# Kernel tuning notes

Measured on AMD Instinct MI355X. Metric: run time of the kernel, lower is better.

Reference implementation:

```python
import jax, jax.numpy as jnp
import numpy as np

B, S, T = 4, 512, 512
V, D, F, H, DK, N = 32000, 512, 2048, 8, 64, 6
PAD = 0

# sinusoidal positional encoding table, matching the torch source exactly
_pos = np.arange(max(S, T))[:, None]
_i = np.arange(D // 2)[None, :]
_ang = _pos / (10000.0 ** (2 * _i / D))
_pe = np.empty((max(S, T), D), dtype=np.float32)
_pe[:, 0::2] = np.sin(_ang)
_pe[:, 1::2] = np.cos(_ang)
PE = jnp.asarray(_pe)


def setup_inputs() -> dict:
    key = jax.random.key(0)
    ks = iter(jax.random.split(key, 64))
    s = 0.02
    w = lambda shape: jax.random.normal(next(ks), shape, jnp.float32) * s
    inp = {
        'src': jax.random.randint(next(ks), (B, S), 0, V, jnp.int32),
        'trg': jax.random.randint(next(ks), (B, T), 0, V, jnp.int32),
        'emb_src': w((V, D)).at[PAD].set(0.0),
        'emb_trg': w((V, D)).at[PAD].set(0.0),
        # encoder stacks (leading axis = layer)
        'enc_wq': w((N, D, H * DK)), 'enc_wk': w((N, D, H * DK)),
        'enc_wv': w((N, D, H * DK)), 'enc_wo': w((N, H * DK, D)),
        'enc_ln1_g': jnp.ones((N, D)), 'enc_ln1_b': jnp.zeros((N, D)),
        'enc_w1': w((N, D, F)), 'enc_b1': jnp.zeros((N, F)),
        'enc_w2': w((N, F, D)), 'enc_b2': jnp.zeros((N, D)),
        'enc_ln2_g': jnp.ones((N, D)), 'enc_ln2_b': jnp.zeros((N, D)),
        # decoder stacks
        'dec_wq': w((N, D, H * DK)), 'dec_wk': w((N, D, H * DK)),
        'dec_wv': w((N, D, H * DK)), 'dec_wo': w((N, H * DK, D)),
        'dec_ln1_g': jnp.ones((N, D)), 'dec_ln1_b': jnp.zeros((N, D)),
        'dec_cq': w((N, D, H * DK)), 'dec_ck': w((N, D, H * DK)),
        'dec_cv': w((N, D, H * DK)), 'dec_co': w((N, H * DK, D)),
        'dec_ln2_g': jnp.ones((N, D)), 'dec_ln2_b': jnp.zeros((N, D)),
        'dec_w1': w((N, D, F)), 'dec_b1': jnp.zeros((N, F)),
        'dec_w2': w((N, F, D)), 'dec_b2': jnp.zeros((N, D)),
        'dec_ln3_g': jnp.ones((N, D)), 'dec_ln3_b': jnp.zeros((N, D)),
        'proj': w((D, V)),
    }
    return inp


def _ln(x, g, b, eps=1e-5):
    m = x.mean(-1, keepdims=True)
    v = ((x - m) ** 2).mean(-1, keepdims=True)
    return (x - m) * jax.lax.rsqrt(v + eps) * g + b


def _mha(xq, xkv, wq, wk, wv, wo, mask):
    b, lq, _ = xq.shape
    lk = xkv.shape[1]
    q = (xq @ wq).reshape(b, lq, H, DK).transpose(0, 2, 1, 3)   # bhqd
    k = (xkv @ wk).reshape(b, lk, H, DK).transpose(0, 2, 1, 3)  # bhkd
    v = (xkv @ wv).reshape(b, lk, H, DK).transpose(0, 2, 1, 3)  # bhkd
    scores = jnp.einsum('bhqd,bhkd->bhqk', q, k)
    scores = jnp.where(mask, -jnp.inf, scores)
    attn = jax.nn.softmax(scores * (DK ** -0.5), axis=-1)
    out = jnp.einsum('bhqk,bhkd->bhqd', attn, v)
    out = out.transpose(0, 2, 1, 3).reshape(b, lq, H * DK)
    return out @ wo


def _ffn(x, w1, b1, w2, b2):
    return jax.nn.relu(x @ w1 + b1) @ w2 + b2


def reference(src, trg, emb_src, emb_trg,
              enc_wq, enc_wk, enc_wv, enc_wo, enc_ln1_g, enc_ln1_b,
              enc_w1, enc_b1, enc_w2, enc_b2, enc_ln2_g, enc_ln2_b,
              dec_wq, dec_wk, dec_wv, dec_wo, dec_ln1_g, dec_ln1_b,
              dec_cq, dec_ck, dec_cv, dec_co, dec_ln2_g, dec_ln2_b,
              dec_w1, dec_b1, dec_w2, dec_b2, dec_ln3_g, dec_ln3_b,
              proj):
    scale = D ** 0.5
    src_pad = (src == PAD)[:, None, None, :]                 # [B,1,1,S]
    trg_pad = (trg == PAD)[:, None, None, :]                 # [B,1,1,T]
    causal = jnp.triu(jnp.ones((T, T), bool), 1)[None, None]  # [1,1,T,T]
    trg_mask = trg_pad | causal

    # encoder (dropout = identity in eval)
    x = emb_src[src] * scale + PE[None, :S]

    def enc_step(h, p):
        wq, wk, wv, wo, g1, b1, w1, bb1, w2, bb2, g2, b2 = p
        h = _ln(h + _mha(h, h, wq, wk, wv, wo, src_pad), g1, b1)
        h = _ln(h + _ffn(h, w1, bb1, w2, bb2), g2, b2)
        return h, None

    x_enc, _ = jax.lax.scan(enc_step, x,
        (enc_wq, enc_wk, enc_wv, enc_wo, enc_ln1_g, enc_ln1_b,
         enc_w1, enc_b1, enc_w2, enc_b2, enc_ln2_g, enc_ln2_b))

    # decoder
    y = emb_trg[trg] * scale + PE[None, :T]

    def dec_step(h, p):
        (wq, wk, wv, wo, g1, b1, cq, ck, cv, co, g2, b2,
         w1, bb1, w2, bb2, g3, b3) = p
        h = _ln(h + _mha(h, h, wq, wk, wv, wo, trg_mask), g1, b1)
        h = _ln(h + _mha(h, x_enc, cq, ck, cv, co, src_pad), g2, b2)
        h = _ln(h + _ffn(h, w1, bb1, w2, bb2), g3, b3)
        return h, None

    y, _ = jax.lax.scan(dec_step, y,
        (dec_wq, dec_wk, dec_wv, dec_wo, dec_ln1_g, dec_ln1_b,
         dec_cq, dec_ck, dec_cv, dec_co, dec_ln2_g, dec_ln2_b,
         dec_w1, dec_b1, dec_w2, dec_b2, dec_ln3_g, dec_ln3_b))

    return y @ proj  # [B, T, trg_vocab]
```

## Files before the change

### kernel.cpp

```cpp
#include <hip/hip_runtime.h>
#include <math.h>

#define BBATCH 4
#define SS 512
#define DDIM 512
#define FFN 2048
#define NHEAD 8
#define DHEAD 64
#define NL 6
#define NVOC 32000
#define MTOK (BBATCH*SS)
#define PAD_ID 0
#define MSZE ((size_t)MTOK * DDIM)

typedef unsigned short u16;
typedef __attribute__((ext_vector_type(8))) short short8;
typedef __attribute__((ext_vector_type(4))) float f32x4;

__device__ __forceinline__ u16 f2bf(float f) {
    union { float f; unsigned u; } v; v.f = f;
    unsigned r = ((v.u >> 16) & 1u) + 0x7fffu;
    return (u16)((v.u + r) >> 16);
}

__device__ __forceinline__ void gload16(const u16* g, u16* l) {
    __builtin_amdgcn_global_load_lds(
        (const __attribute__((address_space(1))) void*)g,
        (__attribute__((address_space(3))) void*)l, 16, 0, 0);
}

template<int N> __device__ __forceinline__ void waitv() {
    if constexpr (N == 0)      asm volatile("s_waitcnt vmcnt(0)" ::: "memory");
    else if constexpr (N == 2) asm volatile("s_waitcnt vmcnt(2)" ::: "memory");
    else if constexpr (N == 4) asm volatile("s_waitcnt vmcnt(4)" ::: "memory");
    else if constexpr (N == 8) asm volatile("s_waitcnt vmcnt(8)" ::: "memory");
    __builtin_amdgcn_sched_barrier(0);
}
__device__ __forceinline__ void rawbar() {
    __builtin_amdgcn_s_barrier();
    __builtin_amdgcn_sched_barrier(0);
}

template<int BM, int BN, int OUTBF, int RELU, int BIAS>
__device__ __forceinline__ void gemm_core(
    u16* __restrict__ AsB, u16* __restrict__ BsB,
    const u16* __restrict__ A, int lda,
    const u16* __restrict__ B, int ldb,
    void* __restrict__ Cv, int ldc,
    int row0, int col0, int K, const float* __restrict__ bias)
{
    const int tid  = threadIdx.x;
    const int lane = tid & 63;
    const int wid  = tid >> 6;
    const int wr   = wid >> 1, wc = wid & 1;
    constexpr int MF = BM / 32, NF = BN / 32, RA = BM / 64, RB = BN / 64;
    constexpr int LPT = RA + RB;

    const u16* aSrc[RA]; int aOff[RA];
    #pragma unroll
    for (int r = 0; r < RA; r++) {
        int row = (tid >> 2) + r * 64;
        int slot = ((tid & 3) << 4) ^ ((row & 3) << 4);
        aSrc[r] = A + (size_t)(row0 + row) * lda + (slot >> 1);
        aOff[r] = r * 2048 + tid * 8;
    }
    const u16* bSrc[RB]; int bOff[RB];
    #pragma unroll
    for (int r = 0; r < RB; r++) {
        int row = (tid >> 2) + r * 64;
        int slot = ((tid & 3) << 4) ^ ((row & 3) << 4);
        bSrc[r] = B + (size_t)(col0 + row) * ldb + (slot >> 1);
        bOff[r] = r * 2048 + tid * 8;
    }

    f32x4 acc[MF][NF];
    const f32x4 zero = {0.f, 0.f, 0.f, 0.f};
    #pragma unroll
    for (int m = 0; m < MF; m++)
        #pragma unroll
        for (int n = 0; n < NF; n++) acc[m][n] = zero;

    auto issue = [&](int t) {
        u16* ad = AsB + (t & 3) * (BM * 32);
        u16* bd = BsB + (t & 3) * (BN * 32);
        #pragma unroll
        for (int r = 0; r < RA; r++) gload16(aSrc[r] + t * 32, ad + aOff[r]);
        #pragma unroll
        for (int r = 0; r < RB; r++) gload16(bSrc[r] + t * 32, bd + bOff[r]);
    };
    auto comp = [&](int t) {
        const u16* as = AsB + (t & 3) * (BM * 32);
        const u16* bs = BsB + (t & 3) * (BN * 32);
        short8 af[MF], bf[NF];
        #pragma unroll
        for (int m = 0; m < MF; m++) {
            int row = wr * (BM / 2) + m * 16 + (lane & 15);
            int slot = ((lane >> 4) << 4) ^ ((row & 3) << 4);
            af[m] = *(const short8*)&as[row * 32 + (slot >> 1)];
        }
        #pragma unroll
        for (int n = 0; n < NF; n++) {
            int row = wc * (BN / 2) + n * 16 + (lane & 15);
            int slot = ((lane >> 4) << 4) ^ ((row & 3) << 4);
            bf[n] = *(const short8*)&bs[row * 32 + (slot >> 1)];
        }
        __builtin_amdgcn_s_setprio(1);
        #pragma unroll
        for (int m = 0; m < MF; m++)
            #pragma unroll
            for (int n = 0; n < NF; n++)
                acc[m][n] = __builtin_amdgcn_mfma_f32_16x16x32_bf16(af[m], bf[n], acc[m][n], 0, 0, 0);
        __builtin_amdgcn_s_setprio(0);
    };

    const int nt = K / 32;
    issue(0); issue(1); issue(2);
    int t = 0;
    for (; t < nt - 2; ++t) {
        waitv<2 * LPT>();
        rawbar();
        if (t + 3 < nt) issue(t + 3);
        comp(t);
    }
    waitv<LPT>(); rawbar(); comp(nt - 2);
    waitv<0>();   rawbar(); comp(nt - 1);

    const int crow = row0 + wr * (BM / 2);
    const int ccol = col0 + wc * (BN / 2);
    #pragma unroll
    for (int m = 0; m < MF; m++) {
        #pragma unroll
        for (int n = 0; n < NF; n++) {
            int col = ccol + n * 16 + (lane & 15);
            float bv = BIAS ? bias[col] : 0.0f;
            #pragma unroll
            for (int i = 0; i < 4; i++) {
                int row = crow + m * 16 + ((lane >> 4) << 2) + i;
                float v = acc[m][n][i] + bv;
                if (RELU) v = fmaxf(v, 0.0f);
                if (OUTBF) ((u16*)Cv)[(size_t)row * ldc + col] = f2bf(v);
                else       ((float*)Cv)[(size_t)row * ldc + col] = v;
            }
        }
    }
}

template<int BM, int BN, int OUTBF, int RELU, int BIAS, int SWZ = 0>
__global__ __launch_bounds__(256) void mgemm(
    const u16* __restrict__ A, int lda, size_t aSb, size_t aSh,
    const u16* __restrict__ B, int ldb, size_t bSb, size_t bSh,
    void* __restrict__ Cv, int ldc, size_t cSb, size_t cSh,
    int K, const float* __restrict__ bias)
{
    __shared__ __align__(16) u16 As[4 * BM * 32];
    __shared__ __align__(16) u16 Bs[4 * BN * 32];
    int bx = blockIdx.x, by = blockIdx.y;
    if (SWZ) {
        int nwg = gridDim.x * gridDim.y;
        int lin = by * gridDim.x + bx;
        int cpx = nwg >> 3;
        int s = (lin & 7) * cpx + (lin >> 3);
        bx = s % gridDim.x; by = s / gridDim.x;
    }
    const int zb = blockIdx.z >> 3, zh = blockIdx.z & 7;
    const u16* Ab = A + (size_t)zb * aSb + (size_t)zh * aSh;
    const u16* Bb = B + (size_t)zb * bSb + (size_t)zh * bSh;
    void* Cb = OUTBF ? (void*)((u16*)Cv + (size_t)zb * cSb + (size_t)zh * cSh)
                     : (void*)((float*)Cv + (size_t)zb * cSb + (size_t)zh * cSh);
    gemm_core<BM, BN, OUTBF, RELU, BIAS>(As, Bs, Ab, lda, Bb, ldb, Cb, ldc,
                                          by * BM, bx * BN, K, bias);
}

template<int BM, int BN>
__global__ __launch_bounds__(256) void mgemm_dual(
    const u16* __restrict__ A1, int lda1, const u16* __restrict__ B1, int ldb1,
    u16* __restrict__ C1, int ldc1, int nx1, int nblk1,
    const u16* __restrict__ A2, int lda2, const u16* __restrict__ B2, int ldb2,
    u16* __restrict__ C2, int ldc2, int nx2,
    int K)
{
    __shared__ __align__(16) u16 As[4 * BM * 32];
    __shared__ __align__(16) u16 Bs[4 * BN * 32];
    int id = blockIdx.x;
    if (id < nblk1) {
        gemm_core<BM, BN, 1, 0, 0>(As, Bs, A1, lda1, B1, ldb1, C1, ldc1,
                                    (id / nx1) * BM, (id % nx1) * BN, K, nullptr);
    } else {
        id -= nblk1;
        gemm_core<BM, BN, 1, 0, 0>(As, Bs, A2, lda2, B2, ldb2, C2, ldc2,
                                    (id / nx2) * BM, (id % nx2) * BN, K, nullptr);
    }
}

template<int CAUSAL>
__global__ __launch_bounds__(256) void flash_attn(
    const u16* __restrict__ Qp, int ldq,
    const u16* __restrict__ Kp, int ldk,
    const u16* __restrict__ Vtp,
    u16* __restrict__ O,
    const int* __restrict__ ids)
{
    __shared__ __align__(16) u16 Kl[3][64 * 64];
    __shared__ __align__(16) u16 Vl[3][64 * 64];
    __shared__ __align__(16) u16 Pl[4][16 * 64];
    __shared__ float msk[SS];

    const int tid = threadIdx.x, lane = tid & 63, wid = tid >> 6;
    const int qt = blockIdx.x, bh = blockIdx.y;
    const int b = bh >> 3, h = bh & 7;
    const int q0 = qt * 64;

    for (int i = tid; i < SS; i += 256)
        msk[i] = (ids[b * SS + i] == PAD_ID) ? -1e30f : 0.0f;

    const int qloc = wid * 16 + (lane & 15);
    const u16* Qb = Qp + (size_t)(b * SS + q0 + qloc) * ldq + h * 64 + ((lane >> 4) * 8);
    short8 qf[2];
    qf[0] = *(const short8*)(Qb);
    qf[1] = *(const short8*)(Qb + 32);

    const u16* Kb = Kp + (size_t)b * SS * ldk + h * 64;
    const u16* Vb = Vtp + (size_t)(h * 64) * MTOK + b * SS;

    auto stage = [&](int buf, int kt) {
        int row = tid >> 3, sl = tid & 7;
        #pragma unroll
        for (int r = 0; r < 2; r++) {
            int rr = row + r * 32;
            int ls = sl ^ (rr & 7);
            gload16(Kb + (size_t)(kt * 64 + rr) * ldk + ls * 8, &Kl[buf][rr * 64 + sl * 8]);
            gload16(Vb + (size_t)rr * MTOK + kt * 64 + ls * 8, &Vl[buf][rr * 64 + sl * 8]);
        }
    };

    const int nt = CAUSAL ? (qt + 1) : (SS / 64);

    float m_i[4], l_i[4];
    f32x4 o_acc[4];
    const f32x4 zero = {0.f, 0.f, 0.f, 0.f};
    #pragma unroll
    for (int i = 0; i < 4; i++) { m_i[i] = -1e30f; l_i[i] = 0.0f; }
    #pragma unroll
    for (int n = 0; n < 4; n++) o_acc[n] = zero;

    auto comp = [&](int kt) {
        const int cur = kt % 3;
        f32x4 s_acc[4];
        #pragma unroll
        for (int n = 0; n < 4; n++) s_acc[n] = zero;
        __builtin_amdgcn_s_setprio(1);
        #pragma unroll
        for (int kk = 0; kk < 2; kk++) {
            #pragma unroll
            for (int n = 0; n < 4; n++) {
                int row = n * 16 + (lane & 15);
                int ls = (kk * 4 + (lane >> 4)) ^ (row & 7);
                short8 kf = *(const short8*)&Kl[cur][row * 64 + ls * 8];
                s_acc[n] = __builtin_amdgcn_mfma_f32_16x16x32_bf16(qf[kk], kf, s_acc[n], 0, 0, 0);
            }
        }
        __builtin_amdgcn_s_setprio(0);

        float sv[4][4];
        #pragma unroll
        for (int n = 0; n < 4; n++) {
            int kg = kt * 64 + n * 16 + (lane & 15);
            float mk = msk[kg];
            #pragma unroll
            for (int i = 0; i < 4; i++) {
                float s = s_acc[n][i] * 0.125f + mk;
                if (CAUSAL) {
                    int qg = q0 + wid * 16 + ((lane >> 4) << 2) + i;
                    if (kg > qg) s = -1e30f;
                }
                sv[n][i] = s;
            }
        }
        float pm[4], mn[4], rs[4], ps[4];
        #pragma unroll
        for (int i = 0; i < 4; i++)
            pm[i] = fmaxf(fmaxf(sv[0][i], sv[1][i]), fmaxf(sv[2][i], sv[3][i]));
        #pragma unroll
        for (int i = 0; i < 4; i++) {
            #pragma unroll
            for (int msh = 1; msh <= 8; msh <<= 1)
                pm[i] = fmaxf(pm[i], __shfl_xor(pm[i], msh));
            mn[i] = fmaxf(m_i[i], pm[i]);
            rs[i] = __expf(m_i[i] - mn[i]);
            m_i[i] = mn[i];
        }
        float p[4][4];
        #pragma unroll
        for (int n = 0; n < 4; n++)
            #pragma unroll
            for (int i = 0; i < 4; i++)
                p[n][i] = (sv[n][i] < -1e29f) ? 0.0f : __expf(sv[n][i] - mn[i]);
        #pragma unroll
        for (int i = 0; i < 4; i++) {
            ps[i] = p[0][i] + p[1][i] + p[2][i] + p[3][i];
            #pragma unroll
            for (int msh = 1; msh <= 8; msh <<= 1)
                ps[i] += __shfl_xor(ps[i], msh);
            l_i[i] = l_i[i] * rs[i] + ps[i];
        }
        #pragma unroll
        for (int n = 0; n < 4; n++)
            #pragma unroll
            for (int i = 0; i < 4; i++)
                o_acc[n][i] *= rs[i];

        #pragma unroll
        for (int n = 0; n < 4; n++) {
            int k = n * 16 + (lane & 15);
            #pragma unroll
            for (int i = 0; i < 4; i++) {
                int q = ((lane >> 4) << 2) + i;
                Pl[wid][q * 64 + (((k >> 3) ^ (q & 7)) << 3) + (k & 7)] = f2bf(p[n][i]);
            }
        }
        asm volatile("s_waitcnt lgkmcnt(0)" ::: "memory");
        __builtin_amdgcn_sched_barrier(0);

        __builtin_amdgcn_s_setprio(1);
        #pragma unroll
        for (int kk = 0; kk < 2; kk++) {
            int qrow = lane & 15;
            int lsp = (kk * 4 + (lane >> 4)) ^ (qrow & 7);
            short8 pa = *(const short8*)&Pl[wid][qrow * 64 + lsp * 8];
            #pragma unroll
            for (int nf = 0; nf < 4; nf++) {
                int row = nf * 16 + (lane & 15);
                int vs = (kk * 4 + (lane >> 4)) ^ (row & 7);
                short8 vf = *(const short8*)&Vl[cur][row * 64 + vs * 8];
                o_acc[nf] = __builtin_amdgcn_mfma_f32_16x16x32_bf16(pa, vf, o_acc[nf], 0, 0, 0);
            }
        }
        __builtin_amdgcn_s_setprio(0);
    };

    stage(0, 0);
    stage(1, 1);
    int t = 0;
    for (; t < nt - 1; ++t) {
        waitv<4>();
        rawbar();
        if (t + 2 < nt) stage((t + 2) % 3, t + 2);
        comp(t);
    }
    waitv<0>(); rawbar(); comp(nt - 1);

    #pragma unroll
    for (int nf = 0; nf < 4; nf++) {
        int d = h * 64 + nf * 16 + (lane & 15);
        #pragma unroll
        for (int i = 0; i < 4; i++) {
            int qg = b * SS + q0 + wid * 16 + ((lane >> 4) << 2) + i;
            O[(size_t)qg * DDIM + d] = f2bf(o_acc[nf][i] / l_i[i]);
        }
    }
}

__device__ __forceinline__ void transp_core(const float* __restrict__ src, u16* __restrict__ dst,
                                            int N, int K, int n0, int k0)
{
    __shared__ u16 t[64][65];
    const int tid = threadIdx.x;
    #pragma unroll
    for (int i = 0; i < 16; i++) {
        int idx = tid + i * 256;
        int kr = idx >> 6, nc = idx & 63;
        t[kr][nc] = f2bf(src[(size_t)(k0 + kr) * N + n0 + nc]);
    }
    __syncthreads();
    #pragma unroll
    for (int i = 0; i < 16; i++) {
        int idx = tid + i * 256;
        int nr = idx >> 6, kc = idx & 63;
        dst[(size_t)(n0 + nr) * K + k0 + kc] = t[kc][nr];
    }
}

__global__ __launch_bounds__(256) void transp(const float* __restrict__ src, u16* __restrict__ dst,
                                              int N, int K, size_t sStride, size_t dStride)
{
    transp_core(src + (size_t)blockIdx.z * sStride, dst + (size_t)blockIdx.z * dStride,
                N, K, blockIdx.x * 64, blockIdx.y * 64);
}

#define OFF_QK 0u
#define OFF_WV 524288u
#define OFF_WO 786432u
#define OFF_CQ 1048576u
#define OFF_CK 1310720u
#define OFF_CV 1572864u
#define OFF_CO 1835008u
#define OFF_W1 2097152u
#define OFF_W2 3145728u
#define WBLK   4194304u
#define M2CNT  262144u
#define MF1CNT 1048576u

__global__ __launch_bounds__(256) void transpW(
    const float* p0, const float* p1, const float* p2, const float* p3,
    const float* p4, const float* p5, const float* p6, const float* p7,
    const float* p8, const float* p9, const float* p10, const float* p11,
    u16* __restrict__ wreg)
{
    int z = blockIdx.z;
    int w = z % 12, l = z / 12;
    const float* ptrs[12] = {p0,p1,p2,p3,p4,p5,p6,p7,p8,p9,p10,p11};
    const float* src = ptrs[w] + (size_t)l * M2CNT;
    u16* dst = wreg + (w < 4 ? (size_t)l * WBLK + (size_t)w * M2CNT
                             : (size_t)(NL + l) * WBLK + (size_t)(w - 4) * M2CNT);
    transp_core(src, dst, 512, 512, blockIdx.x * 64, blockIdx.y * 64);
}

__global__ __launch_bounds__(256) void transpF1(const float* __restrict__ e,
                                                const float* __restrict__ d, u16* __restrict__ wreg)
{
    int z = blockIdx.z; int l = z % NL, w = z / NL;
    const float* src = (w ? d : e) + (size_t)l * MF1CNT;
    u16* dst = wreg + (size_t)(w * NL + l) * WBLK + OFF_W1;
    transp_core(src, dst, 2048, 512, blockIdx.x * 64, blockIdx.y * 64);
}

__global__ __launch_bounds__(256) void transpF2(const float* __restrict__ e,
                                                const float* __restrict__ d, u16* __restrict__ wreg)
{
    int z = blockIdx.z; int l = z % NL, w = z / NL;
    const float* src = (w ? d : e) + (size_t)l * MF1CNT;
    u16* dst = wreg + (size_t)(w * NL + l) * WBLK + OFF_W2;
    transp_core(src, dst, 512, 2048, blockIdx.x * 64, blockIdx.y * 64);
}

__global__ void embed_kernel(const int* __restrict__ src, const int* __restrict__ trg,
                             const float* __restrict__ es, const float* __restrict__ et,
                             float* __restrict__ X, u16* __restrict__ Xb,
                             float* __restrict__ Y, u16* __restrict__ Ybf)
{
    int gtok = blockIdx.x;
    int d = threadIdx.x;
    bool dec = gtok >= MTOK;
    int tok = dec ? gtok - MTOK : gtok;
    int pos = tok & (SS - 1);
    int id = (dec ? trg : src)[tok];
    const float* emb = dec ? et : es;
    int i = d >> 1;
    double freq = exp(-(2.0 * (double)i / (double)DDIM) * log(10000.0));
    double ang = (double)pos * freq;
    float pe = (float)((d & 1) ? cos(ang) : sin(ang));
    float val = emb[(size_t)id * DDIM + d] * 22.62741699796952f + pe;
    (dec ? Y : X)[(size_t)tok * DDIM + d] = val;
    (dec ? Ybf : Xb)[(size_t)tok * DDIM + d] = f2bf(val);
}

__global__ __launch_bounds__(256) void add_ln_kernel(float* __restrict__ x,
    const float* __restrict__ addv, const float* __restrict__ g,
    const float* __restrict__ bta, u16* __restrict__ xb)
{
    int row = blockIdx.x;
    int tid = threadIdx.x;
    size_t base = (size_t)row * DDIM;
    __shared__ float sbuf[4];

    float v0 = x[base + tid]       + addv[base + tid];
    float v1 = x[base + tid + 256] + addv[base + tid + 256];

    float s = v0 + v1;
    #pragma unroll
    for (int o = 32; o > 0; o >>= 1) s += __shfl_down(s, o);
    if ((tid & 63) == 0) sbuf[tid >> 6] = s;
    __syncthreads();
    float mean = (sbuf[0] + sbuf[1] + sbuf[2] + sbuf[3]) * (1.0f / DDIM);
    __syncthreads();

    float d0 = v0 - mean, d1 = v1 - mean;
    float ss = d0 * d0 + d1 * d1;
    #pragma unroll
    for (int o = 32; o > 0; o >>= 1) ss += __shfl_down(ss, o);
    if ((tid & 63) == 0) sbuf[tid >> 6] = ss;
    __syncthreads();
    float var = (sbuf[0] + sbuf[1] + sbuf[2] + sbuf[3]) * (1.0f / DDIM);
    float inv = rsqrtf(var + 1e-5f);

    float o0 = d0 * inv * g[tid]       + bta[tid];
    float o1 = d1 * inv * g[tid + 256] + bta[tid + 256];
    x[base + tid] = o0;
    x[base + tid + 256] = o1;
    xb[base + tid] = f2bf(o0);
    xb[base + tid + 256] = f2bf(o1);
}

__global__ __launch_bounds__(256) void add_ln_red(float* __restrict__ x,
    const float* __restrict__ part, const float* __restrict__ bias,
    const float* __restrict__ g, const float* __restrict__ bta, u16* __restrict__ xb)
{
    int row = blockIdx.x;
    int tid = threadIdx.x;
    size_t base = (size_t)row * DDIM;
    __shared__ float sbuf[4];

    float v0 = x[base + tid]       + bias[tid];
    float v1 = x[base + tid + 256] + bias[tid + 256];
    #pragma unroll
    for (int s4 = 0; s4 < 4; s4++) {
        v0 += part[s4 * MSZE + base + tid];
        v1 += part[s4 * MSZE + base + tid + 256];
    }

    float s = v0 + v1;
    #pragma unroll
    for (int o = 32; o > 0; o >>= 1) s += __shfl_down(s, o);
    if ((tid & 63) == 0) sbuf[tid >> 6] = s;
    __syncthreads();
    float mean = (sbuf[0] + sbuf[1] + sbuf[2] + sbuf[3]) * (1.0f / DDIM);
    __syncthreads();

    float d0 = v0 - mean, d1 = v1 - mean;
    float ss = d0 * d0 + d1 * d1;
    #pragma unroll
    for (int o = 32; o > 0; o >>= 1) ss += __shfl_down(ss, o);
    if ((tid & 63) == 0) sbuf[tid >> 6] = ss;
    __syncthreads();
    float var = (sbuf[0] + sbuf[1] + sbuf[2] + sbuf[3]) * (1.0f / DDIM);
    float inv = rsqrtf(var + 1e-5f);

    float o0 = d0 * inv * g[tid]       + bta[tid];
    float o1 = d1 * inv * g[tid + 256] + bta[tid + 256];
    x[base + tid] = o0;
    x[base + tid + 256] = o1;
    xb[base + tid] = f2bf(o0);
    xb[base + tid + 256] = f2bf(o1);
}

extern "C" void kernel_launch(void* const* d_in, const int* in_sizes, int n_in,
                              void* d_out, int out_size, void* d_ws, size_t ws_size,
                              hipStream_t stream)
{
    (void)in_sizes; (void)n_in; (void)out_size;

    const int*   src      = (const int*)  d_in[0];
    const int*   trg      = (const int*)  d_in[1];
    const float* emb_src  = (const float*)d_in[2];
    const float* emb_trg  = (const float*)d_in[3];
    const float* enc_wq   = (const float*)d_in[4];
    const float* enc_wk   = (const float*)d_in[5];
    const float* enc_wv   = (const float*)d_in[6];
    const float* enc_wo   = (const float*)d_in[7];
    const float* enc_ln1g = (const float*)d_in[8];
    const float* enc_ln1b = (const float*)d_in[9];
    const float* enc_w1   = (const float*)d_in[10];
    const float* enc_b1   = (const float*)d_in[11];
    const float* enc_w2   = (const float*)d_in[12];
    const float* enc_b2   = (const float*)d_in[13];
    const float* enc_ln2g = (const float*)d_in[14];
    const float* enc_ln2b = (const float*)d_in[15];
    const float* dec_wq   = (const float*)d_in[16];
    const float* dec_wk   = (const float*)d_in[17];
    const float* dec_wv   = (const float*)d_in[18];
    const float* dec_wo   = (const float*)d_in[19];
    const float* dec_ln1g = (const float*)d_in[20];
    const float* dec_ln1b = (const float*)d_in[21];
    const float* dec_cq   = (const float*)d_in[22];
    const float* dec_ck   = (const float*)d_in[23];
    const float* dec_cv   = (const float*)d_in[24];
    const float* dec_co   = (const float*)d_in[25];
    const float* dec_ln2g = (const float*)d_in[26];
    const float* dec_ln2b = (const float*)d_in[27];
    const float* dec_w1   = (const float*)d_in[28];
    const float* dec_b1   = (const float*)d_in[29];
    const float* dec_w2   = (const float*)d_in[30];
    const float* dec_b2   = (const float*)d_in[31];
    const float* dec_ln3g = (const float*)d_in[32];
    const float* dec_ln3b = (const float*)d_in[33];
    const float* proj     = (const float*)d_in[34];

    float* OUT = (float*)d_out;
    char* base = (char*)d_ws;

    size_t off = 0;
    auto carve = [&](size_t bytes) { char* p = base + off; off += (bytes + 255) & ~(size_t)255; return p; };

    float* X      = (float*)carve(MSZE * 4);
    float* Yb     = (float*)carve(MSZE * 4);
    float* T1     = (float*)carve(MSZE * 4);
    u16*   Xb     = (u16*)  carve(MSZE * 2);
    u16*   Ybf    = (u16*)  carve(MSZE * 2);
    u16*   QKb    = (u16*)  carve((size_t)MTOK * 1024 * 2);
    u16*   Vt     = (u16*)  carve((size_t)512 * MTOK * 2);
    u16*   CTX    = (u16*)  carve(MSZE * 2);
    u16*   HFF    = (u16*)  carve((size_t)MTOK * FFN * 2);
    u16*   Kcr    = (u16*)  carve((size_t)NL * MTOK * 512 * 2);
    u16*   Vtc    = (u16*)  carve((size_t)NL * 512 * MTOK * 2);
    u16*   projT  = (u16*)  carve((size_t)NVOC * 512 * 2);
    float* Tp4    = (float*)carve((size_t)4 * MSZE * 4);

    const size_t WFULL_B = (size_t)12 * WBLK * 2;
    bool full = (ws_size >= off + WFULL_B);
    u16* Wreg = (u16*)carve(full ? WFULL_B : (size_t)WBLK * 2);

    auto T = [&](const float* s, u16* d, int Kd, int Nd, size_t ss, size_t ds, int L) {
        transp<<<dim3(Nd / 64, Kd / 64, L), 256, 0, stream>>>(s, d, Nd, Kd, ss, ds);
    };

    T(proj, projT, 512, NVOC, 0, 0, 1);
    if (full) {
        transpW<<<dim3(8, 8, 12 * NL), 256, 0, stream>>>(
            enc_wq, enc_wk, enc_wv, enc_wo,
            dec_wq, dec_wk, dec_wv, dec_wo,
            dec_cq, dec_ck, dec_cv, dec_co, Wreg);
        transpF1<<<dim3(32, 8, 2 * NL), 256, 0, stream>>>(enc_w1, dec_w1, Wreg);
        transpF2<<<dim3(8, 32, 2 * NL), 256, 0, stream>>>(enc_w2, dec_w2, Wreg);
    }
    embed_kernel<<<2 * MTOK, DDIM, 0, stream>>>(src, trg, emb_src, emb_trg, X, Xb, Yb, Ybf);

    auto self_attn = [&](const u16* xsrc, const u16* wb, const int* mask_ids, int causal) {
        mgemm_dual<64, 64><<<dim3(768), 256, 0, stream>>>(
            xsrc, 512, wb + OFF_QK, 512, QKb, 1024, 16, 512,
            wb + OFF_WV, 512, xsrc, 512, Vt, MTOK, 32,
            512);
        if (causal)
            flash_attn<1><<<dim3(8, 32), 256, 0, stream>>>(QKb, 1024, QKb + 512, 1024, Vt, CTX, mask_ids);
        else
            flash_attn<0><<<dim3(8, 32), 256, 0, stream>>>(QKb, 1024, QKb + 512, 1024, Vt, CTX, mask_ids);
        mgemm<64, 64, 0, 0, 0><<<dim3(8, 32, 1), 256, 0, stream>>>(
            CTX, 512, 0, 0, wb + OFF_WO, 512, 0, 0, T1, 512, 0, 0, 512, nullptr);
    };

    auto ffn = [&](const u16* xsrc, const u16* wb, const float* b1) {
        mgemm<64, 64, 1, 1, 1><<<dim3(32, 32, 1), 256, 0, stream>>>(
            xsrc, 512, 0, 0, wb + OFF_W1, 512, 0, 0, HFF, FFN, 0, 0, 512, b1);
        mgemm<64, 64, 0, 0, 0><<<dim3(8, 32, 4), 256, 0, stream>>>(
            HFF, 2048, 0, 512, wb + OFF_W2, 2048, 0, 512,
            Tp4, 512, 0, MSZE, 512, nullptr);
    };

    const size_t M2 = M2CNT, MF1 = MF1CNT;

    for (int l = 0; l < NL; l++) {
        u16* wb;
        if (full) wb = Wreg + (size_t)l * WBLK;
        else {
            wb = Wreg;
            T(enc_wq + l * M2,  wb + OFF_QK,      512, 512,  0, 0, 1);
            T(enc_wk + l * M2,  wb + OFF_QK + M2, 512, 512,  0, 0, 1);
            T(enc_wv + l * M2,  wb + OFF_WV,      512, 512,  0, 0, 1);
            T(enc_wo + l * M2,  wb + OFF_WO,      512, 512,  0, 0, 1);
            T(enc_w1 + l * MF1, wb + OFF_W1,      512, 2048, 0, 0, 1);
            T(enc_w2 + l * MF1, wb + OFF_W2,      2048, 512, 0, 0, 1);
        }
        self_attn(Xb, wb, src, 0);
        add_ln_kernel<<<MTOK, 256, 0, stream>>>(X, T1, enc_ln1g + l * DDIM, enc_ln1b + l * DDIM, Xb);
        ffn(Xb, wb, enc_b1 + l * FFN);
        add_ln_red<<<MTOK, 256, 0, stream>>>(X, Tp4, enc_b2 + l * DDIM,
                                             enc_ln2g + l * DDIM, enc_ln2b + l * DDIM, Xb);
    }

    if (full) {
        u16* Wd = Wreg + (size_t)NL * WBLK;
        mgemm<64, 64, 1, 0, 0><<<dim3(8, 32, NL), 256, 0, stream>>>(
            Xb, 512, 0, 0, Wd + OFF_CK, 512, 0, WBLK, Kcr, 512, 0, (size_t)MTOK * 512, 512, nullptr);
        mgemm<64, 64, 1, 0, 0><<<dim3(32, 8, NL), 256, 0, stream>>>(
            Wd + OFF_CV, 512, 0, WBLK, Xb, 512, 0, 0, Vtc, MTOK, 0, (size_t)512 * MTOK, 512, nullptr);
    }

    for (int l = 0; l < NL; l++) {
        u16* wb;
        if (full) wb = Wreg + (size_t)(NL + l) * WBLK;
        else {
            wb = Wreg;
            T(dec_wq + l * M2,  wb + OFF_QK,      512, 512,  0, 0, 1);
            T(dec_wk + l * M2,  wb + OFF_QK + M2, 512, 512,  0, 0, 1);
            T(dec_wv + l * M2,  wb + OFF_WV,      512, 512,  0, 0, 1);
            T(dec_wo + l * M2,  wb + OFF_WO,      512, 512,  0, 0, 1);
            T(dec_cq + l * M2,  wb + OFF_CQ,      512, 512,  0, 0, 1);
            T(dec_ck + l * M2,  wb + OFF_CK,      512, 512,  0, 0, 1);
            T(dec_cv + l * M2,  wb + OFF_CV,      512, 512,  0, 0, 1);
            T(dec_co + l * M2,  wb + OFF_CO,      512, 512,  0, 0, 1);
            T(dec_w1 + l * MF1, wb + OFF_W1,      512, 2048, 0, 0, 1);
            T(dec_w2 + l * MF1, wb + OFF_W2,      2048, 512, 0, 0, 1);
            mgemm<64, 64, 1, 0, 0><<<dim3(8, 32, 1), 256, 0, stream>>>(
                Xb, 512, 0, 0, wb + OFF_CK, 512, 0, 0, Kcr + (size_t)l * MTOK * 512, 512, 0, 0, 512, nullptr);
            mgemm<64, 64, 1, 0, 0><<<dim3(32, 8, 1), 256, 0, stream>>>(
                wb + OFF_CV, 512, 0, 0, Xb, 512, 0, 0, Vtc + (size_t)l * 512 * MTOK, MTOK, 0, 0, 512, nullptr);
        }
        self_attn(Ybf, wb, trg, 1);
        add_ln_kernel<<<MTOK, 256, 0, stream>>>(Yb, T1, dec_ln1g + l * DDIM, dec_ln1b + l * DDIM, Ybf);
        mgemm<64, 64, 1, 0, 0><<<dim3(8, 32, 1), 256, 0, stream>>>(
            Ybf, 512, 0, 0, wb + OFF_CQ, 512, 0, 0, QKb, 1024, 0, 0, 512, nullptr);
        flash_attn<0><<<dim3(8, 32), 256, 0, stream>>>(
            QKb, 1024, Kcr + (size_t)l * MTOK * 512, 512, Vtc + (size_t)l * 512 * MTOK, CTX, src);
        mgemm<64, 64, 0, 0, 0><<<dim3(8, 32, 1), 256, 0, stream>>>(
            CTX, 512, 0, 0, wb + OFF_CO, 512, 0, 0, T1, 512, 0, 0, 512, nullptr);
        add_ln_kernel<<<MTOK, 256, 0, stream>>>(Yb, T1, dec_ln2g + l * DDIM, dec_ln2b + l * DDIM, Ybf);
        ffn(Ybf, wb, dec_b1 + l * FFN);
        add_ln_red<<<MTOK, 256, 0, stream>>>(Yb, Tp4, dec_b2 + l * DDIM,
                                             dec_ln3g + l * DDIM, dec_ln3b + l * DDIM, Ybf);
    }

    mgemm<128, 128, 0, 0, 0, 1><<<dim3(NVOC / 128, 16, 1), 256, 0, stream>>>(
        Ybf, 512, 0, 0, projT, 512, 0, 0, OUT, NVOC, 0, 0, 512, nullptr);
}
```

Measured before the change: 1.473 ms.

## Fuse decoder LN into cross-Q GEMM, merge transposes, enlarge GEMM tiles

Adds gemm_lnA, which computes the decoder's first add+LayerNorm inside the cross-attention Q projection, keeping the normalized A tile in LDS. The LN is applied a second time in add_ln2_kernel, which fuses both residual LNs into one pass. All weight transposes, including proj, are merged into one launch. The QKV, FFN1 and FFN2 GEMMs move to 128x64 tiles. Together these aim to cut launches and intermediate traffic. The costs are redundant LN work in each of the 8 column blocks of gemm_lnA, a scalar serial LN loop, one-pass variance with reduced precision, and fewer blocks in flight.

Result: slower. 1.677 ms (+13.8%).

```diff
diff --git a/kernel.cpp b/kernel.cpp
--- a/kernel.cpp
+++ b/kernel.cpp
@@ -31,8 +31,11 @@
 
 template<int N> __device__ __forceinline__ void waitv() {
     if constexpr (N == 0)      asm volatile("s_waitcnt vmcnt(0)" ::: "memory");
+    else if constexpr (N == 1) asm volatile("s_waitcnt vmcnt(1)" ::: "memory");
     else if constexpr (N == 2) asm volatile("s_waitcnt vmcnt(2)" ::: "memory");
+    else if constexpr (N == 3) asm volatile("s_waitcnt vmcnt(3)" ::: "memory");
     else if constexpr (N == 4) asm volatile("s_waitcnt vmcnt(4)" ::: "memory");
+    else if constexpr (N == 6) asm volatile("s_waitcnt vmcnt(6)" ::: "memory");
     else if constexpr (N == 8) asm volatile("s_waitcnt vmcnt(8)" ::: "memory");
     __builtin_amdgcn_sched_barrier(0);
 }
@@ -190,6 +193,103 @@
         gemm_core<BM, BN, 1, 0, 0>(As, Bs, A2, lda2, B2, ldb2, C2, ldc2,
                                     (id / nx2) * BM, (id % nx2) * BN, K, nullptr);
     }
+}
+
+__global__ __launch_bounds__(256) void gemm_lnA(
+    const float* __restrict__ Yf, const float* __restrict__ T1f,
+    const u16* __restrict__ Bw,
+    u16* __restrict__ Cout, int ldc,
+    const float* __restrict__ g, const float* __restrict__ bta)
+{
+    __shared__ __align__(16) u16 Al[64 * 512];
+    __shared__ __align__(16) u16 Bl[3 * 64 * 32];
+
+    const int tid = threadIdx.x, lane = tid & 63, wid = tid >> 6;
+    const int wr = wid >> 1, wc = wid & 1;
+    const int row0 = blockIdx.y * 64, col0 = blockIdx.x * 64;
+    const int l15 = lane & 15, l4 = lane >> 4;
+
+    const int brow = tid >> 2;
+    const int bslot = ((tid & 3) << 4) ^ ((brow & 3) << 4);
+    const u16* bSrc = Bw + (size_t)(col0 + brow) * 512 + (bslot >> 1);
+    const int bOff = tid * 8;
+    auto issueB = [&](int t) {
+        gload16(bSrc + t * 32, Bl + (t % 3) * 2048 + bOff);
+    };
+    issueB(0); issueB(1);
+
+    {
+        const int row = tid >> 2, q = tid & 3;
+        const size_t gb = (size_t)(row0 + row) * DDIM + q * 128;
+        float s = 0.f, ss = 0.f;
+        for (int j = 0; j < 128; j++) {
+            float v = Yf[gb + j] + T1f[gb + j];
+            s += v; ss += v * v;
+        }
+        s  += __shfl_xor(s, 1);  s  += __shfl_xor(s, 2);
+        ss += __shfl_xor(ss, 1); ss += __shfl_xor(ss, 2);
+        float mean = s * (1.0f / DDIM);
+        float var  = ss * (1.0f / DDIM) - mean * mean;
+        float inv  = rsqrtf(var + 1e-5f);
+        for (int j = 0; j < 128; j++) {
+            int c = q * 128 + j;
+            float v = Yf[gb + j] + T1f[gb + j];
+            float o = (v - mean) * inv * g[c] + bta[c];
+            int sl = c >> 3, e = c & 7;
+            int phys = (sl & ~3) | ((sl & 3) ^ (row & 3));
+            Al[row * 512 + phys * 8 + e] = f2bf(o);
+        }
+    }
+    __syncthreads();
+
+    f32x4 acc[2][2];
+    const f32x4 zero = {0.f, 0.f, 0.f, 0.f};
+    #pragma unroll
+    for (int m = 0; m < 2; m++)
+        #pragma unroll
+        for (int n = 0; n < 2; n++) acc[m][n] = zero;
+
+    for (int t = 0; t < 16; ++t) {
+        if (t < 15) { waitv<1>(); } else { waitv<0>(); }
+        rawbar();
+        if (t + 2 < 16) issueB(t + 2);
+        const u16* bs = Bl + (t % 3) * 2048;
+        short8 af[2], bf[2];
+        #pragma unroll
+        for (int m = 0; m < 2; m++) {
+            int row = wr * 32 + m * 16 + l15;
+            int phys = (t * 4) | (l4 ^ (row & 3));
+            af[m] = *(const short8*)&Al[row * 512 + phys * 8];
+        }
+        #pragma unroll
+        for (int n = 0; n < 2; n++) {
+            int row = wc * 32 + n * 16 + l15;
+            int slot = (l4 << 4) ^ ((row & 3) << 4);
+            bf[n] = *(const short8*)&bs[row * 32 + (slot >> 1)];
+        }
+        __builtin_amdgcn_s_setprio(1);
+        #pragma unroll
+        for (int m = 0; m < 2; m++)
+            #pragma unroll
+            for (int n = 0; n < 2; n++)
+                acc[m][n] = __builtin_amdgcn_mfma_f32_16x16x32_bf16(af[m], bf[n], acc[m][n], 0, 0, 0);
+        __builtin_amdgcn_s_setprio(0);
+        rawbar();
+    }
+
+    const int crow = row0 + wr * 32;
+    const int ccol = col0 + wc * 32;
+    #pragma unroll
+    for (int m = 0; m < 2; m++)
+        #pragma unroll
+        for (int n = 0; n < 2; n++) {
+            int col = ccol + n * 16 + l15;
+            #pragma unroll
+            for (int i = 0; i < 4; i++) {
+                int row = crow + m * 16 + (l4 << 2) + i;
+                Cout[(size_t)row * ldc + col] = f2bf(acc[m][n][i]);
+            }
+        }
 }
 
 template<int CAUSAL>
@@ -400,6 +500,42 @@
 #define M2CNT  262144u
 #define MF1CNT 1048576u
 
+__global__ __launch_bounds__(256) void transp_all(
+    const float* p0, const float* p1, const float* p2, const float* p3,
+    const float* p4, const float* p5, const float* p6, const float* p7,
+    const float* p8, const float* p9, const float* p10, const float* p11,
+    const float* ew1, const float* dw1, const float* ew2, const float* dw2,
+    const float* proj, u16* __restrict__ wreg, u16* __restrict__ projT)
+{
+    int jid = blockIdx.x;
+    if (jid < 4608) {
+        int z = jid >> 6, t = jid & 63;
+        int w = z % 12, l = z / 12;
+        const float* ptrs[12] = {p0,p1,p2,p3,p4,p5,p6,p7,p8,p9,p10,p11};
+        const float* src = ptrs[w] + (size_t)l * M2CNT;
+        u16* dst = wreg + (w < 4 ? (size_t)l * WBLK + (size_t)w * M2CNT
+                                 : (size_t)(NL + l) * WBLK + (size_t)(w - 4) * M2CNT);
+        transp_core(src, dst, 512, 512, (t & 7) * 64, (t >> 3) * 64);
+    } else if (jid < 7680) {
+        int j = jid - 4608;
+        int z = j >> 8, t = j & 255;
+        int l = z % NL, w = z / NL;
+        const float* src = (w ? dw1 : ew1) + (size_t)l * MF1CNT;
+        u16* dst = wreg + (size_t)(w * NL + l) * WBLK + OFF_W1;
+        transp_core(src, dst, 2048, 512, (t % 32) * 64, (t / 32) * 64);
+    } else if (jid < 10752) {
+        int j = jid - 7680;
+        int z = j >> 8, t = j & 255;
+        int l = z % NL, w = z / NL;
+        const float* src = (w ? dw2 : ew2) + (size_t)l * MF1CNT;
+        u16* dst = wreg + (size_t)(w * NL + l) * WBLK + OFF_W2;
+        transp_core(src, dst, 512, 2048, (t % 8) * 64, (t / 8) * 64);
+    } else {
+        int j = jid - 10752;
+        transp_core(proj, projT, NVOC, 512, (j % 500) * 64, (j / 500) * 64);
+    }
+}
+
 __global__ __launch_bounds__(256) void transpW(
     const float* p0, const float* p1, const float* p2, const float* p3,
     const float* p4, const float* p5, const float* p6, const float* p7,
@@ -413,24 +549,6 @@
     u16* dst = wreg + (w < 4 ? (size_t)l * WBLK + (size_t)w * M2CNT
                              : (size_t)(NL + l) * WBLK + (size_t)(w - 4) * M2CNT);
     transp_core(src, dst, 512, 512, blockIdx.x * 64, blockIdx.y * 64);
-}
-
-__global__ __launch_bounds__(256) void transpF1(const float* __restrict__ e,
-                                                const float* __restrict__ d, u16* __restrict__ wreg)
-{
-    int z = blockIdx.z; int l = z % NL, w = z / NL;
-    const float* src = (w ? d : e) + (size_t)l * MF1CNT;
-    u16* dst = wreg + (size_t)(w * NL + l) * WBLK + OFF_W1;
-    transp_core(src, dst, 2048, 512, blockIdx.x * 64, blockIdx.y * 64);
-}
-
-__global__ __launch_bounds__(256) void transpF2(const float* __restrict__ e,
-                                                const float* __restrict__ d, u16* __restrict__ wreg)
-{
-    int z = blockIdx.z; int l = z % NL, w = z / NL;
-    const float* src = (w ? d : e) + (size_t)l * MF1CNT;
-    u16* dst = wreg + (size_t)(w * NL + l) * WBLK + OFF_W2;
-    transp_core(src, dst, 512, 2048, blockIdx.x * 64, blockIdx.y * 64);
 }
 
 __global__ void embed_kernel(const int* __restrict__ src, const int* __restrict__ trg,
@@ -485,6 +603,63 @@
 
     float o0 = d0 * inv * g[tid]       + bta[tid];
     float o1 = d1 * inv * g[tid + 256] + bta[tid + 256];
+    x[base + tid] = o0;
+    x[base + tid + 256] = o1;
+    xb[base + tid] = f2bf(o0);
+    xb[base + tid + 256] = f2bf(o1);
+}
+
+__global__ __launch_bounds__(256) void add_ln2_kernel(float* __restrict__ x,
+    const float* __restrict__ T1, const float* __restrict__ T2,
+    const float* __restrict__ g1, const float* __restrict__ b1,
+    const float* __restrict__ g2, const float* __restrict__ b2,
+    u16* __restrict__ xb)
+{
+    int row = blockIdx.x;
+    int tid = threadIdx.x;
+    size_t base = (size_t)row * DDIM;
+    __shared__ float sbuf[4];
+
+    float v0 = x[base + tid]       + T1[base + tid];
+    float v1 = x[base + tid + 256] + T1[base + tid + 256];
+    float s = v0 + v1;
+    #pragma unroll
+    for (int o = 32; o > 0; o >>= 1) s += __shfl_down(s, o);
+    if ((tid & 63) == 0) sbuf[tid >> 6] = s;
+    __syncthreads();
+    float mean = (sbuf[0] + sbuf[1] + sbuf[2] + sbuf[3]) * (1.0f / DDIM);
+    __syncthreads();
+    float d0 = v0 - mean, d1 = v1 - mean;
+    float ss = d0 * d0 + d1 * d1;
+    #pragma unroll
+    for (int o = 32; o > 0; o >>= 1) ss += __shfl_down(ss, o);
+    if ((tid & 63) == 0) sbuf[tid >> 6] = ss;
+    __syncthreads();
+    float var = (sbuf[0] + sbuf[1] + sbuf[2] + sbuf[3]) * (1.0f / DDIM);
+    float inv = rsqrtf(var + 1e-5f);
+    float l0 = d0 * inv * g1[tid]       + b1[tid];
+    float l1 = d1 * inv * g1[tid + 256] + b1[tid + 256];
+    __syncthreads();
+
+    float w0 = l0 + T2[base + tid];
+    float w1 = l1 + T2[base + tid + 256];
+    s = w0 + w1;
+    #pragma unroll
+    for (int o = 32; o > 0; o >>= 1) s += __shfl_down(s, o);
+    if ((tid & 63) == 0) sbuf[tid >> 6] = s;
+    __syncthreads();
+    mean = (sbuf[0] + sbuf[1] + sbuf[2] + sbuf[3]) * (1.0f / DDIM);
+    __syncthreads();
+    d0 = w0 - mean; d1 = w1 - mean;
+    ss = d0 * d0 + d1 * d1;
+    #pragma unroll
+    for (int o = 32; o > 0; o >>= 1) ss += __shfl_down(ss, o);
+    if ((tid & 63) == 0) sbuf[tid >> 6] = ss;
+    __syncthreads();
+    var = (sbuf[0] + sbuf[1] + sbuf[2] + sbuf[3]) * (1.0f / DDIM);
+    inv = rsqrtf(var + 1e-5f);
+    float o0 = d0 * inv * g2[tid]       + b2[tid];
+    float o1 = d1 * inv * g2[tid + 256] + b2[tid + 256];
     x[base + tid] = o0;
     x[base + tid + 256] = o1;
     xb[base + tid] = f2bf(o0);
@@ -584,6 +759,7 @@
     float* X      = (float*)carve(MSZE * 4);
     float* Yb     = (float*)carve(MSZE * 4);
     float* T1     = (float*)carve(MSZE * 4);
+    float* T2     = (float*)carve(MSZE * 4);
     u16*   Xb     = (u16*)  carve(MSZE * 2);
     u16*   Ybf    = (u16*)  carve(MSZE * 2);
     u16*   QKb    = (u16*)  carve((size_t)MTOK * 1024 * 2);
@@ -603,20 +779,21 @@
         transp<<<dim3(Nd / 64, Kd / 64, L), 256, 0, stream>>>(s, d, Nd, Kd, ss, ds);
     };
 
-    T(proj, projT, 512, NVOC, 0, 0, 1);
     if (full) {
-        transpW<<<dim3(8, 8, 12 * NL), 256, 0, stream>>>(
+        transp_all<<<dim3(14752), 256, 0, stream>>>(
             enc_wq, enc_wk, enc_wv, enc_wo,
             dec_wq, dec_wk, dec_wv, dec_wo,
-            dec_cq, dec_ck, dec_cv, dec_co, Wreg);
-        transpF1<<<dim3(32, 8, 2 * NL), 256, 0, stream>>>(enc_w1, dec_w1, Wreg);
-        transpF2<<<dim3(8, 32, 2 * NL), 256, 0, stream>>>(enc_w2, dec_w2, Wreg);
+            dec_cq, dec_ck, dec_cv, dec_co,
+            enc_w1, dec_w1, enc_w2, dec_w2,
+            proj, Wreg, projT);
+    } else {
+        T(proj, projT, 512, NVOC, 0, 0, 1);
     }
     embed_kernel<<<2 * MTOK, DDIM, 0, stream>>>(src, trg, emb_src, emb_trg, X, Xb, Yb, Ybf);
 
-    auto self_attn = [&](const u16* xsrc, const u16* wb, const int* mask_ids, int causal) {
-        mgemm_dual<64, 64><<<dim3(768), 256, 0, stream>>>(
-            xsrc, 512, wb + OFF_QK, 512, QKb, 1024, 16, 512,
+    auto self_attn = [&](const u16* xsrc, const u16* wb, const int* mask_ids, int causal, float* outT) {
+        mgemm_dual<128, 64><<<dim3(384), 256, 0, stream>>>(
+            xsrc, 512, wb + OFF_QK, 512, QKb, 1024, 16, 256,
             wb + OFF_WV, 512, xsrc, 512, Vt, MTOK, 32,
             512);
         if (causal)
@@ -624,13 +801,13 @@
         else
             flash_attn<0><<<dim3(8, 32), 256, 0, stream>>>(QKb, 1024, QKb + 512, 1024, Vt, CTX, mask_ids);
         mgemm<64, 64, 0, 0, 0><<<dim3(8, 32, 1), 256, 0, stream>>>(
-            CTX, 512, 0, 0, wb + OFF_WO, 512, 0, 0, T1, 512, 0, 0, 512, nullptr);
+            CTX, 512, 0, 0, wb + OFF_WO, 512, 0, 0, outT, 512, 0, 0, 512, nullptr);
     };
 
     auto ffn = [&](const u16* xsrc, const u16* wb, const float* b1) {
-        mgemm<64, 64, 1, 1, 1><<<dim3(32, 32, 1), 256, 0, stream>>>(
+        mgemm<128, 64, 1, 1, 1><<<dim3(32, 16, 1), 256, 0, stream>>>(
             xsrc, 512, 0, 0, wb + OFF_W1, 512, 0, 0, HFF, FFN, 0, 0, 512, b1);
-        mgemm<64, 64, 0, 0, 0><<<dim3(8, 32, 4), 256, 0, stream>>>(
+        mgemm<128, 64, 0, 0, 0><<<dim3(8, 16, 4), 256, 0, stream>>>(
             HFF, 2048, 0, 512, wb + OFF_W2, 2048, 0, 512,
             Tp4, 512, 0, MSZE, 512, nullptr);
     };
@@ -649,7 +826,7 @@
             T(enc_w1 + l * MF1, wb + OFF_W1,      512, 2048, 0, 0, 1);
             T(enc_w2 + l * MF1, wb + OFF_W2,      2048, 512, 0, 0, 1);
         }
-        self_attn(Xb, wb, src, 0);
+        self_attn(Xb, wb, src, 0, T1);
         add_ln_kernel<<<MTOK, 256, 0, stream>>>(X, T1, enc_ln1g + l * DDIM, enc_ln1b + l * DDIM, Xb);
         ffn(Xb, wb, enc_b1 + l * FFN);
         add_ln_red<<<MTOK, 256, 0, stream>>>(X, Tp4, enc_b2 + l * DDIM,
@@ -684,15 +861,16 @@
             mgemm<64, 64, 1, 0, 0><<<dim3(32, 8, 1), 256, 0, stream>>>(
                 wb + OFF_CV, 512, 0, 0, Xb, 512, 0, 0, Vtc + (size_t)l * 512 * MTOK, MTOK, 0, 0, 512, nullptr);
         }
-        self_attn(Ybf, wb, trg, 1);
-        add_ln_kernel<<<MTOK, 256, 0, stream>>>(Yb, T1, dec_ln1g + l * DDIM, dec_ln1b + l * DDIM, Ybf);
-        mgemm<64, 64, 1, 0, 0><<<dim3(8, 32, 1), 256, 0, stream>>>(
-            Ybf, 512, 0, 0, wb + OFF_CQ, 512, 0, 0, QKb, 1024, 0, 0, 512, nullptr);
+        self_attn(Ybf, wb, trg, 1, T1);
+        gemm_lnA<<<dim3(8, 32), 256, 0, stream>>>(
+            Yb, T1, wb + OFF_CQ, QKb, 1024, dec_ln1g + l * DDIM, dec_ln1b + l * DDIM);
         flash_attn<0><<<dim3(8, 32), 256, 0, stream>>>(
             QKb, 1024, Kcr + (size_t)l * MTOK * 512, 512, Vtc + (size_t)l * 512 * MTOK, CTX, src);
         mgemm<64, 64, 0, 0, 0><<<dim3(8, 32, 1), 256, 0, stream>>>(
-            CTX, 512, 0, 0, wb + OFF_CO, 512, 0, 0, T1, 512, 0, 0, 512, nullptr);
-        add_ln_kernel<<<MTOK, 256, 0, stream>>>(Yb, T1, dec_ln2g + l * DDIM, dec_ln2b + l * DDIM, Ybf);
+            CTX, 512, 0, 0, wb + OFF_CO, 512, 0, 0, T2, 512, 0, 0, 512, nullptr);
+        add_ln2_kernel<<<MTOK, 256, 0, stream>>>(Yb, T1, T2,
+            dec_ln1g + l * DDIM, dec_ln1b + l * DDIM,
+            dec_ln2g + l * DDIM, dec_ln2b + l * DDIM, Ybf);
         ffn(Ybf, wb, dec_b1 + l * FFN);
         add_ln_red<<<MTOK, 256, 0, stream>>>(Yb, Tp4, dec_b2 + l * DDIM,
                                              dec_ln3g + l * DDIM, dec_ln3b + l * DDIM, Ybf);
```
